# Optimization experiments

Measured on AMD Instinct MI355X. Metric: run time of the kernel, lower is better.

Reference implementation:

```python
import jax, jax.numpy as jnp
import numpy as np

D_MODEL = 2048
HEAD_DIM = 128

def setup_inputs() -> dict:
    key = jax.random.key(0)
    ks = jax.random.split(key, 7)
    s = 1.0 / np.sqrt(D_MODEL)
    x = jax.random.normal(ks[0], (4, 4096, D_MODEL), dtype=jnp.float32)
    Wq = jax.random.uniform(ks[1], (D_MODEL, HEAD_DIM), jnp.float32, -s, s)
    bq = jax.random.uniform(ks[2], (HEAD_DIM,), jnp.float32, -s, s)
    Wk = jax.random.uniform(ks[3], (D_MODEL, HEAD_DIM), jnp.float32, -s, s)
    bk = jax.random.uniform(ks[4], (HEAD_DIM,), jnp.float32, -s, s)
    Wv = jax.random.uniform(ks[5], (D_MODEL, HEAD_DIM), jnp.float32, -s, s)
    bv = jax.random.uniform(ks[6], (HEAD_DIM,), jnp.float32, -s, s)
    return {"x": x, "Wq": Wq, "bq": bq, "Wk": Wk, "bk": bk, "Wv": Wv, "bv": bv}

def reference(x, Wq, bq, Wk, bk, Wv, bv):
    # x: [B, T, d_model]
    B, T, _ = x.shape
    q = jnp.einsum('btd,dh->bth', x, Wq) + bq  # [B,T,H]
    k = jnp.einsum('btd,dh->bth', x, Wk) + bk
    v = jnp.einsum('btd,dh->bth', x, Wv) + bv
    scores = jnp.einsum('bth,bsh->bts', q, k) / jnp.sqrt(jnp.float32(HEAD_DIM))  # [B,T,T]
    causal = jnp.tril(jnp.ones((T, T), dtype=bool))
    scores = jnp.where(causal[None], scores, -jnp.inf)
    probs = jax.nn.softmax(scores, axis=-1)
    return jnp.einsum('bts,bsh->bth', probs, v)  # [B,T,H]
```

## Files before the change

kernel.cpp:

```cpp
#include <hip/hip_runtime.h>
#include <math.h>

#define D_MODEL 2048
#define HD      128
#define NB      4
#define TT      4096
#define M_TOT   (NB * TT)
#define NCH     160
#define CHT     16

typedef __attribute__((ext_vector_type(8))) short bf16x8;
typedef __attribute__((ext_vector_type(4))) float f32x4;

__device__ __forceinline__ ushort f2bf(float f) {
    union { float f; unsigned int u; } v; v.f = f;
    unsigned int u = v.u;
    unsigned int r = (u + 0x7FFFu + ((u >> 16) & 1u)) >> 16;
    return (ushort)r;
}

__device__ __forceinline__ void gload_lds16(const void* g, void* l) {
    __builtin_amdgcn_global_load_lds(
        (const __attribute__((address_space(1))) unsigned int*)g,
        (__attribute__((address_space(3))) unsigned int*)l, 16, 0, 0);
}

__global__ void wt_kernel(const float* __restrict__ Wq, const float* __restrict__ Wk,
                          const float* __restrict__ Wv, ushort* __restrict__ WT) {
    int p = blockIdx.y;
    const float* W = (p == 0) ? Wq : ((p == 1) ? Wk : Wv);
    int e = blockIdx.x * 256 + threadIdx.x;
    int n = e & 127;
    int k = e >> 7;
    WT[(size_t)p * (128 * 2048) + (size_t)n * 2048 + k] = f2bf(W[(size_t)k * 128 + n]);
}

__global__ __launch_bounds__(256) void proj_fused(
        const float* __restrict__ x, const ushort* __restrict__ WT,
        const float* __restrict__ bq, const float* __restrict__ bk, const float* __restrict__ bv,
        ushort* __restrict__ Qb, ushort* __restrict__ Kb, ushort* __restrict__ Vt) {
    const int bx   = blockIdx.x;
    const int row0 = (bx >> 1) * 64;
    const int col0 = (bx & 1) * 192;

    __shared__ ushort As[64 * 40];
    __shared__ ushort Bs[192 * 32];

    const int tid  = threadIdx.x;
    const int lane = tid & 63;
    const int wv   = tid >> 6;
    const int rw   = wv >> 1;
    const int cw   = wv & 1;
    const int quad = lane >> 4;
    const int ln16 = lane & 15;

    size_t  boff[3];
    ushort* bdst[3];
    for (int i = 0; i < 3; i++) {
        int c = i * 256 + tid;
        int n = c >> 2, j = c & 3;
        int kc = j ^ ((n >> 1) & 3);
        boff[i] = (size_t)(col0 + n) * 2048 + kc * 8;
        bdst[i] = &Bs[(i * 256 + wv * 64) * 8];
    }
    int arow[2], acol[2];
    for (int j = 0; j < 2; j++) {
        int c = j * 256 + tid;
        arow[j] = c >> 3;
        acol[j] = (c & 7) * 4;
    }

    f32x4 acc[2][6];
    for (int m2 = 0; m2 < 2; m2++)
        for (int nt = 0; nt < 6; nt++)
            acc[m2][nt] = (f32x4){0.f, 0.f, 0.f, 0.f};

    float4 areg[2];
    for (int j = 0; j < 2; j++)
        areg[j] = *(const float4*)(x + (size_t)(row0 + arow[j]) * D_MODEL + acol[j]);

    for (int k0 = 0; k0 < D_MODEL; k0 += 32) {
        __syncthreads();
        for (int i = 0; i < 3; i++)
            gload_lds16(WT + boff[i] + k0, bdst[i]);
        for (int j = 0; j < 2; j++) {
            ushort4 o;
            o.x = f2bf(areg[j].x); o.y = f2bf(areg[j].y);
            o.z = f2bf(areg[j].z); o.w = f2bf(areg[j].w);
            *(ushort4*)&As[arow[j] * 40 + acol[j]] = o;
        }
        __syncthreads();
        if (k0 + 32 < D_MODEL)
            for (int j = 0; j < 2; j++)
                areg[j] = *(const float4*)(x + (size_t)(row0 + arow[j]) * D_MODEL + k0 + 32 + acol[j]);

        bf16x8 a[2], b[6];
        for (int m2 = 0; m2 < 2; m2++)
            a[m2] = *(const bf16x8*)&As[(rw * 32 + m2 * 16 + ln16) * 40 + quad * 8];
        for (int nt = 0; nt < 6; nt++) {
            int n = cw * 96 + nt * 16 + ln16;
            b[nt] = *(const bf16x8*)&Bs[n * 32 + (quad ^ ((n >> 1) & 3)) * 8];
        }
        for (int m2 = 0; m2 < 2; m2++)
            for (int nt = 0; nt < 6; nt++)
                acc[m2][nt] = __builtin_amdgcn_mfma_f32_16x16x32_bf16(a[m2], b[nt], acc[m2][nt], 0, 0, 0);
    }

    for (int nt = 0; nt < 6; nt++) {
        int col = col0 + cw * 96 + nt * 16 + ln16;
        int p = col >> 7;
        int h = col & 127;
        const float* bias = (p == 0) ? bq : ((p == 1) ? bk : bv);
        float bc = bias[h];
        for (int m2 = 0; m2 < 2; m2++) {
            int rbase = row0 + rw * 32 + m2 * 16 + quad * 4;
            if (p < 2) {
                ushort* O = (p == 0) ? Qb : Kb;
                for (int r = 0; r < 4; r++)
                    O[(size_t)(rbase + r) * HD + h] = f2bf(acc[m2][nt][r] + bc);
            } else {
                int b = rbase >> 12;
                int t = rbase & 4095;
                ushort4 o;
                o.x = f2bf(acc[m2][nt][0] + bc);
                o.y = f2bf(acc[m2][nt][1] + bc);
                o.z = f2bf(acc[m2][nt][2] + bc);
                o.w = f2bf(acc[m2][nt][3] + bc);
                *(ushort4*)(Vt + ((size_t)b * HD + h) * TT + t) = o;
            }
        }
    }
}

#define SCALE 0.08838834764831845f

__global__ __launch_bounds__(256, 4) void attn_part(
        const ushort* __restrict__ Qb, const ushort* __restrict__ Kb,
        const ushort* __restrict__ Vt, float* __restrict__ Opart,
        float* __restrict__ Mpart, float* __restrict__ Lpart) {
    const int blk = blockIdx.x;
    const int bb  = blk & 3;
    const int cid = blk >> 2;

    int rem = cid, qt = 63;
    for (;;) {
        int cnt = (qt >> 4) + 1;
        if (rem < cnt) break;
        rem -= cnt; --qt;
    }
    const int ch    = rem;
    const int st_lo = ch * CHT;
    const int st_hi = min(qt + 1, st_lo + CHT);
    const int q0    = qt * 64;

    __shared__ ushort Ks[64 * 128];
    __shared__ ushort Vs[128 * 64];
    __shared__ ushort Ps[64 * 64];

    const int tid  = threadIdx.x;
    const int lane = tid & 63;
    const int wv   = tid >> 6;
    const int quad = lane >> 4;
    const int ln16 = lane & 15;
    const int sw8  = ln16 & 7;

    bf16x8 qf[4];
    {
        const ushort* qrow = Qb + (size_t)(bb * TT + q0 + 16 * wv + ln16) * HD;
        for (int kc = 0; kc < 4; kc++)
            qf[kc] = *(const bf16x8*)(qrow + kc * 32 + quad * 8);
    }

    int koff[4], voff[4];
    ushort *kdst[4], *vdst[4];
    for (int i = 0; i < 4; i++) {
        int c = i * 256 + tid;
        { int r = c >> 4, j = c & 15, kc = j ^ (r & 15);
          koff[i] = r * HD + kc * 8; }
        { int h = c >> 3, j = c & 7, kc = j ^ (h & 7);
          voff[i] = h * TT + kc * 8; }
        kdst[i] = &Ks[(i * 256 + wv * 64) * 8];
        vdst[i] = &Vs[(i * 256 + wv * 64) * 8];
    }

    f32x4 o_acc[8];
    for (int nt = 0; nt < 8; nt++) o_acc[nt] = (f32x4){0.f, 0.f, 0.f, 0.f};
    float m_i[4], l_i[4];
    for (int r = 0; r < 4; r++) { m_i[r] = -INFINITY; l_i[r] = 0.f; }

    for (int st = st_lo; st < st_hi; st++) {
        const int s0 = st * 64;
        __syncthreads();
        const ushort* kbase = Kb + ((size_t)bb * TT + s0) * HD;
        const ushort* vbase = Vt + (size_t)bb * HD * TT + s0;
        for (int i = 0; i < 4; i++) gload_lds16(kbase + koff[i], kdst[i]);
        for (int i = 0; i < 4; i++) gload_lds16(vbase + voff[i], vdst[i]);
        __syncthreads();

        f32x4 sacc[4];
        for (int nt = 0; nt < 4; nt++) sacc[nt] = (f32x4){0.f, 0.f, 0.f, 0.f};
        for (int kc = 0; kc < 4; kc++) {
            int lc = kc * 4 + quad;
            for (int nt = 0; nt < 4; nt++) {
                int r = nt * 16 + ln16;
                bf16x8 b = *(const bf16x8*)&Ks[r * 128 + (lc ^ ln16) * 8];
                sacc[nt] = __builtin_amdgcn_mfma_f32_16x16x32_bf16(qf[kc], b, sacc[nt], 0, 0, 0);
            }
        }

        const bool diag = (st == qt);
        float mx[4];
        for (int r = 0; r < 4; r++) {
            for (int nt = 0; nt < 4; nt++) {
                float s = sacc[nt][r] * SCALE;
                if (diag) {
                    int sg = s0 + nt * 16 + ln16;
                    int qg = q0 + 16 * wv + quad * 4 + r;
                    if (sg > qg) s = -INFINITY;
                }
                sacc[nt][r] = s;
            }
            mx[r] = fmaxf(fmaxf(sacc[0][r], sacc[1][r]), fmaxf(sacc[2][r], sacc[3][r]));
        }
        for (int off = 8; off >= 1; off >>= 1)
            for (int r = 0; r < 4; r++)
                mx[r] = fmaxf(mx[r], __shfl_xor(mx[r], off));

        float al[4];
        for (int r = 0; r < 4; r++) {
            float mnew = fmaxf(m_i[r], mx[r]);
            al[r] = __expf(m_i[r] - mnew);
            m_i[r] = mnew;
        }
        float rs[4];
        for (int r = 0; r < 4; r++) {
            float s = 0.f;
            for (int nt = 0; nt < 4; nt++) {
                float pv = __expf(sacc[nt][r] - m_i[r]);
                sacc[nt][r] = pv;
                s += pv;
            }
            rs[r] = s;
        }
        for (int off = 8; off >= 1; off >>= 1)
            for (int r = 0; r < 4; r++)
                rs[r] += __shfl_xor(rs[r], off);
        for (int r = 0; r < 4; r++) l_i[r] = l_i[r] * al[r] + rs[r];
        for (int nt = 0; nt < 8; nt++)
            for (int r = 0; r < 4; r++)
                o_acc[nt][r] *= al[r];

        for (int nt = 0; nt < 4; nt++)
            for (int r = 0; r < 4; r++) {
                int row = 16 * wv + quad * 4 + r;
                int cj  = nt * 2 + (ln16 >> 3);
                Ps[row * 64 + ((cj ^ (row & 7)) * 8) + sw8] = f2bf(sacc[nt][r]);
            }

        for (int kc2 = 0; kc2 < 2; kc2++) {
            int lc = kc2 * 4 + quad;
            int prow = 16 * wv + ln16;
            bf16x8 a = *(const bf16x8*)&Ps[prow * 64 + ((lc ^ sw8) * 8)];
            for (int nt = 0; nt < 8; nt++) {
                int h = nt * 16 + ln16;
                bf16x8 b = *(const bf16x8*)&Vs[h * 64 + ((lc ^ sw8) * 8)];
                o_acc[nt] = __builtin_amdgcn_mfma_f32_16x16x32_bf16(a, b, o_acc[nt], 0, 0, 0);
            }
        }
    }

    const size_t slot = (size_t)bb * NCH + cid;
    for (int nt = 0; nt < 8; nt++)
        for (int r = 0; r < 4; r++)
            Opart[(slot * 64 + 16 * wv + quad * 4 + r) * HD + nt * 16 + ln16] = o_acc[nt][r];
    if (ln16 == 0)
        for (int r = 0; r < 4; r++) {
            Mpart[slot * 64 + 16 * wv + quad * 4 + r] = m_i[r];
            Lpart[slot * 64 + 16 * wv + quad * 4 + r] = l_i[r];
        }
}

__global__ __launch_bounds__(256) void merge_kernel(
        const float* __restrict__ Opart, const float* __restrict__ Mpart,
        const float* __restrict__ Lpart, float* __restrict__ out) {
    const int qt = blockIdx.x;
    const int bb = blockIdx.y;
    const int nch = (qt >> 4) + 1;
    int base = 0;
    for (int q = 63; q > qt; --q) base += (q >> 4) + 1;

    const int tid = threadIdx.x;
    const int q0  = qt * 64;
    for (int e = tid; e < 64 * 32; e += 256) {
        int row = e >> 5;
        int c4  = e & 31;
        float M = -INFINITY;
        float mv[4];
        for (int ch = 0; ch < nch; ch++) {
            mv[ch] = Mpart[((size_t)bb * NCH + base + ch) * 64 + row];
            M = fmaxf(M, mv[ch]);
        }
        float L = 0.f;
        float w[4];
        for (int ch = 0; ch < nch; ch++) {
            w[ch] = __expf(mv[ch] - M);
            L += w[ch] * Lpart[((size_t)bb * NCH + base + ch) * 64 + row];
        }
        float4 acc = {0.f, 0.f, 0.f, 0.f};
        for (int ch = 0; ch < nch; ch++) {
            const float4 o = *(const float4*)(Opart +
                (((size_t)bb * NCH + base + ch) * 64 + row) * HD + c4 * 4);
            acc.x += w[ch] * o.x; acc.y += w[ch] * o.y;
            acc.z += w[ch] * o.z; acc.w += w[ch] * o.w;
        }
        float invL = 1.f / L;
        float4 res = {acc.x * invL, acc.y * invL, acc.z * invL, acc.w * invL};
        *(float4*)(out + ((size_t)bb * TT + q0 + row) * HD + c4 * 4) = res;
    }
}

extern "C" void kernel_launch(void* const* d_in, const int* in_sizes, int n_in,
                              void* d_out, int out_size, void* d_ws, size_t ws_size,
                              hipStream_t stream) {
    const float* x  = (const float*)d_in[0];
    const float* Wq = (const float*)d_in[1];
    const float* bq = (const float*)d_in[2];
    const float* Wk = (const float*)d_in[3];
    const float* bk = (const float*)d_in[4];
    const float* Wv = (const float*)d_in[5];
    const float* bv = (const float*)d_in[6];
    float* out = (float*)d_out;

    ushort* WT = (ushort*)d_ws;
    ushort* Qb = WT + (size_t)3 * HD * D_MODEL;
    ushort* Kb = Qb + (size_t)M_TOT * HD;
    ushort* Vt = Kb + (size_t)M_TOT * HD;
    float* Opart = (float*)(Vt + (size_t)M_TOT * HD);
    float* Mpart = Opart + (size_t)NB * NCH * 64 * HD;
    float* Lpart = Mpart + (size_t)NB * NCH * 64;

    hipLaunchKernelGGL(wt_kernel, dim3(1024, 3), dim3(256), 0, stream, Wq, Wk, Wv, WT);
    hipLaunchKernelGGL(proj_fused, dim3(512), dim3(256), 0, stream,
                       x, WT, bq, bk, bv, Qb, Kb, Vt);
    hipLaunchKernelGGL(attn_part, dim3(NB * NCH), dim3(256), 0, stream,
                       Qb, Kb, Vt, Opart, Mpart, Lpart);
    hipLaunchKernelGGL(merge_kernel, dim3(64, NB), dim3(256), 0, stream,
                       Opart, Mpart, Lpart, out);
}
```

Before: 332.5 us.

## Double-buffer attention K/V tiles, widen projection K-step, tile weight transpose

The attention kernel now double-buffers its K and V shared-memory tiles, prefetching the next tile while the current one is computed, and drops one barrier per iteration. Its occupancy hint is lowered to make room for the extra LDS. The projection GEMM moves from a 32-wide to a 128-wide K step with larger LDS tiles and a 16-way XOR swizzle, so it synchronizes less often but uses more registers and LDS. The weight transpose kernel now goes through shared memory, giving coalesced 16-byte stores in place of strided 2-byte writes.

```diff
diff --git a/kernel.cpp b/kernel.cpp
--- a/kernel.cpp
+++ b/kernel.cpp
@@ -25,17 +25,31 @@
         (__attribute__((address_space(3))) unsigned int*)l, 16, 0, 0);
 }
 
-__global__ void wt_kernel(const float* __restrict__ Wq, const float* __restrict__ Wk,
-                          const float* __restrict__ Wv, ushort* __restrict__ WT) {
-    int p = blockIdx.y;
+__global__ __launch_bounds__(256) void wt_kernel(
+        const float* __restrict__ Wq, const float* __restrict__ Wk,
+        const float* __restrict__ Wv, ushort* __restrict__ WT) {
+    const int p  = blockIdx.y;
+    const int k0 = blockIdx.x * 128;
     const float* W = (p == 0) ? Wq : ((p == 1) ? Wk : Wv);
-    int e = blockIdx.x * 256 + threadIdx.x;
-    int n = e & 127;
-    int k = e >> 7;
-    WT[(size_t)p * (128 * 2048) + (size_t)n * 2048 + k] = f2bf(W[(size_t)k * 128 + n]);
-}
-
-__global__ __launch_bounds__(256) void proj_fused(
+
+    __shared__ ushort Ts[128 * 136];
+
+    const int tid = threadIdx.x;
+    for (int i = 0; i < 64; i++) {
+        int c  = i * 256 + tid;
+        int kk = c >> 7, n = c & 127;
+        Ts[n * 136 + kk] = f2bf(W[(size_t)(k0 + kk) * 128 + n]);
+    }
+    __syncthreads();
+    for (int i = 0; i < 8; i++) {
+        int c = i * 256 + tid;
+        int n = c >> 4, j = c & 15;
+        *(uint4*)(WT + (size_t)p * (128 * 2048) + (size_t)n * 2048 + k0 + j * 8) =
+            *(const uint4*)&Ts[n * 136 + j * 8];
+    }
+}
+
+__global__ __launch_bounds__(256, 2) void proj_fused(
         const float* __restrict__ x, const ushort* __restrict__ WT,
         const float* __restrict__ bq, const float* __restrict__ bk, const float* __restrict__ bv,
         ushort* __restrict__ Qb, ushort* __restrict__ Kb, ushort* __restrict__ Vt) {
@@ -43,8 +57,8 @@
     const int row0 = (bx >> 1) * 64;
     const int col0 = (bx & 1) * 192;
 
-    __shared__ ushort As[64 * 40];
-    __shared__ ushort Bs[192 * 32];
+    __shared__ ushort As[64 * 136];
+    __shared__ ushort Bs[192 * 128];
 
     const int tid  = threadIdx.x;
     const int lane = tid & 63;
@@ -54,20 +68,20 @@
     const int quad = lane >> 4;
     const int ln16 = lane & 15;
 
-    size_t  boff[3];
-    ushort* bdst[3];
-    for (int i = 0; i < 3; i++) {
+    size_t  boff[12];
+    ushort* bdst[12];
+    for (int i = 0; i < 12; i++) {
         int c = i * 256 + tid;
-        int n = c >> 2, j = c & 3;
-        int kc = j ^ ((n >> 1) & 3);
+        int n = c >> 4, j = c & 15;
+        int kc = j ^ (n & 15);
         boff[i] = (size_t)(col0 + n) * 2048 + kc * 8;
         bdst[i] = &Bs[(i * 256 + wv * 64) * 8];
     }
-    int arow[2], acol[2];
-    for (int j = 0; j < 2; j++) {
-        int c = j * 256 + tid;
-        arow[j] = c >> 3;
-        acol[j] = (c & 7) * 4;
+    int arow[8], apos[8];
+    for (int i = 0; i < 8; i++) {
+        int c = i * 256 + tid;
+        arow[i] = c >> 5;
+        apos[i] = c & 31;
     }
 
     f32x4 acc[2][6];
@@ -75,35 +89,39 @@
         for (int nt = 0; nt < 6; nt++)
             acc[m2][nt] = (f32x4){0.f, 0.f, 0.f, 0.f};
 
-    float4 areg[2];
-    for (int j = 0; j < 2; j++)
-        areg[j] = *(const float4*)(x + (size_t)(row0 + arow[j]) * D_MODEL + acol[j]);
-
-    for (int k0 = 0; k0 < D_MODEL; k0 += 32) {
+    float4 areg[8];
+    for (int i = 0; i < 8; i++)
+        areg[i] = *(const float4*)(x + (size_t)(row0 + arow[i]) * D_MODEL + apos[i] * 4);
+
+    for (int k0 = 0; k0 < D_MODEL; k0 += 128) {
         __syncthreads();
-        for (int i = 0; i < 3; i++)
+        for (int i = 0; i < 12; i++)
             gload_lds16(WT + boff[i] + k0, bdst[i]);
-        for (int j = 0; j < 2; j++) {
+        for (int i = 0; i < 8; i++) {
             ushort4 o;
-            o.x = f2bf(areg[j].x); o.y = f2bf(areg[j].y);
-            o.z = f2bf(areg[j].z); o.w = f2bf(areg[j].w);
-            *(ushort4*)&As[arow[j] * 40 + acol[j]] = o;
+            o.x = f2bf(areg[i].x); o.y = f2bf(areg[i].y);
+            o.z = f2bf(areg[i].z); o.w = f2bf(areg[i].w);
+            *(ushort4*)&As[arow[i] * 136 + apos[i] * 4] = o;
         }
         __syncthreads();
-        if (k0 + 32 < D_MODEL)
-            for (int j = 0; j < 2; j++)
-                areg[j] = *(const float4*)(x + (size_t)(row0 + arow[j]) * D_MODEL + k0 + 32 + acol[j]);
-
-        bf16x8 a[2], b[6];
-        for (int m2 = 0; m2 < 2; m2++)
-            a[m2] = *(const bf16x8*)&As[(rw * 32 + m2 * 16 + ln16) * 40 + quad * 8];
-        for (int nt = 0; nt < 6; nt++) {
-            int n = cw * 96 + nt * 16 + ln16;
-            b[nt] = *(const bf16x8*)&Bs[n * 32 + (quad ^ ((n >> 1) & 3)) * 8];
-        }
-        for (int m2 = 0; m2 < 2; m2++)
-            for (int nt = 0; nt < 6; nt++)
-                acc[m2][nt] = __builtin_amdgcn_mfma_f32_16x16x32_bf16(a[m2], b[nt], acc[m2][nt], 0, 0, 0);
+        if (k0 + 128 < D_MODEL)
+            for (int i = 0; i < 8; i++)
+                areg[i] = *(const float4*)(x + (size_t)(row0 + arow[i]) * D_MODEL
+                                             + k0 + 128 + apos[i] * 4);
+
+        for (int mi = 0; mi < 4; mi++) {
+            bf16x8 a[2], b[6];
+            for (int m2 = 0; m2 < 2; m2++)
+                a[m2] = *(const bf16x8*)&As[(rw * 32 + m2 * 16 + ln16) * 136 + mi * 32 + quad * 8];
+            for (int nt = 0; nt < 6; nt++) {
+                int n = cw * 96 + nt * 16 + ln16;
+                int slot = (mi * 4 + quad) ^ (n & 15);
+                b[nt] = *(const bf16x8*)&Bs[n * 128 + slot * 8];
+            }
+            for (int m2 = 0; m2 < 2; m2++)
+                for (int nt = 0; nt < 6; nt++)
+                    acc[m2][nt] = __builtin_amdgcn_mfma_f32_16x16x32_bf16(a[m2], b[nt], acc[m2][nt], 0, 0, 0);
+        }
     }
 
     for (int nt = 0; nt < 6; nt++) {
@@ -134,7 +152,7 @@
 
 #define SCALE 0.08838834764831845f
 
-__global__ __launch_bounds__(256, 4) void attn_part(
+__global__ __launch_bounds__(256, 2) void attn_part(
         const ushort* __restrict__ Qb, const ushort* __restrict__ Kb,
         const ushort* __restrict__ Vt, float* __restrict__ Opart,
         float* __restrict__ Mpart, float* __restrict__ Lpart) {
@@ -153,8 +171,8 @@
     const int st_hi = min(qt + 1, st_lo + CHT);
     const int q0    = qt * 64;
 
-    __shared__ ushort Ks[64 * 128];
-    __shared__ ushort Vs[128 * 64];
+    __shared__ ushort Ks[2][64 * 128];
+    __shared__ ushort Vs[2][128 * 64];
     __shared__ ushort Ps[64 * 64];
 
     const int tid  = threadIdx.x;
@@ -164,23 +182,28 @@
     const int ln16 = lane & 15;
     const int sw8  = ln16 & 7;
 
-    bf16x8 qf[4];
-    {
-        const ushort* qrow = Qb + (size_t)(bb * TT + q0 + 16 * wv + ln16) * HD;
-        for (int kc = 0; kc < 4; kc++)
-            qf[kc] = *(const bf16x8*)(qrow + kc * 32 + quad * 8);
-    }
-
-    int koff[4], voff[4];
-    ushort *kdst[4], *vdst[4];
+    int koff[4], voff[4], ldso[4];
     for (int i = 0; i < 4; i++) {
         int c = i * 256 + tid;
         { int r = c >> 4, j = c & 15, kc = j ^ (r & 15);
           koff[i] = r * HD + kc * 8; }
         { int h = c >> 3, j = c & 7, kc = j ^ (h & 7);
           voff[i] = h * TT + kc * 8; }
-        kdst[i] = &Ks[(i * 256 + wv * 64) * 8];
-        vdst[i] = &Vs[(i * 256 + wv * 64) * 8];
+        ldso[i] = (i * 256 + wv * 64) * 8;
+    }
+    const ushort* kbase = Kb + (size_t)bb * TT * HD;
+    const ushort* vbase = Vt + (size_t)bb * HD * TT;
+
+    {
+        const int s0 = st_lo * 64;
+        for (int i = 0; i < 4; i++) gload_lds16(kbase + (size_t)s0 * HD + koff[i], &Ks[0][ldso[i]]);
+        for (int i = 0; i < 4; i++) gload_lds16(vbase + s0 + voff[i], &Vs[0][ldso[i]]);
+    }
+    bf16x8 qf[4];
+    {
+        const ushort* qrow = Qb + (size_t)(bb * TT + q0 + 16 * wv + ln16) * HD;
+        for (int kc = 0; kc < 4; kc++)
+            qf[kc] = *(const bf16x8*)(qrow + kc * 32 + quad * 8);
     }
 
     f32x4 o_acc[8];
@@ -188,14 +211,17 @@
     float m_i[4], l_i[4];
     for (int r = 0; r < 4; r++) { m_i[r] = -INFINITY; l_i[r] = 0.f; }
 
+    __syncthreads();
+
     for (int st = st_lo; st < st_hi; st++) {
-        const int s0 = st * 64;
-        __syncthreads();
-        const ushort* kbase = Kb + ((size_t)bb * TT + s0) * HD;
-        const ushort* vbase = Vt + (size_t)bb * HD * TT + s0;
-        for (int i = 0; i < 4; i++) gload_lds16(kbase + koff[i], kdst[i]);
-        for (int i = 0; i < 4; i++) gload_lds16(vbase + voff[i], vdst[i]);
-        __syncthreads();
+        const int s0  = st * 64;
+        const int buf = (st - st_lo) & 1;
+
+        if (st + 1 < st_hi) {
+            const int s1 = s0 + 64;
+            for (int i = 0; i < 4; i++) gload_lds16(kbase + (size_t)s1 * HD + koff[i], &Ks[buf ^ 1][ldso[i]]);
+            for (int i = 0; i < 4; i++) gload_lds16(vbase + s1 + voff[i], &Vs[buf ^ 1][ldso[i]]);
+        }
 
         f32x4 sacc[4];
         for (int nt = 0; nt < 4; nt++) sacc[nt] = (f32x4){0.f, 0.f, 0.f, 0.f};
@@ -203,7 +229,7 @@
             int lc = kc * 4 + quad;
             for (int nt = 0; nt < 4; nt++) {
                 int r = nt * 16 + ln16;
-                bf16x8 b = *(const bf16x8*)&Ks[r * 128 + (lc ^ ln16) * 8];
+                bf16x8 b = *(const bf16x8*)&Ks[buf][r * 128 + ((lc ^ ln16) * 8)];
                 sacc[nt] = __builtin_amdgcn_mfma_f32_16x16x32_bf16(qf[kc], b, sacc[nt], 0, 0, 0);
             }
         }
@@ -263,10 +289,12 @@
             bf16x8 a = *(const bf16x8*)&Ps[prow * 64 + ((lc ^ sw8) * 8)];
             for (int nt = 0; nt < 8; nt++) {
                 int h = nt * 16 + ln16;
-                bf16x8 b = *(const bf16x8*)&Vs[h * 64 + ((lc ^ sw8) * 8)];
+                bf16x8 b = *(const bf16x8*)&Vs[buf][h * 64 + ((lc ^ sw8) * 8)];
                 o_acc[nt] = __builtin_amdgcn_mfma_f32_16x16x32_bf16(a, b, o_acc[nt], 0, 0, 0);
             }
         }
+
+        __syncthreads();
     }
 
     const size_t slot = (size_t)bb * NCH + cid;
@@ -339,7 +367,7 @@
     float* Mpart = Opart + (size_t)NB * NCH * 64 * HD;
     float* Lpart = Mpart + (size_t)NB * NCH * 64;
 
-    hipLaunchKernelGGL(wt_kernel, dim3(1024, 3), dim3(256), 0, stream, Wq, Wk, Wv, WT);
+    hipLaunchKernelGGL(wt_kernel, dim3(16, 3), dim3(256), 0, stream, Wq, Wk, Wv, WT);
     hipLaunchKernelGGL(proj_fused, dim3(512), dim3(256), 0, stream,
                        x, WT, bq, bk, bv, Qb, Kb, Vt);
     hipLaunchKernelGGL(attn_part, dim3(NB * NCH), dim3(256), 0, stream,
```

Result: no change. 332.2 us (-0.1%).
